# Kernel tuning notes

Hardware: AMD Instinct MI355X
Metric: run time of the kernel (lower is better)

The kernel has to match this reference:

```python
import jax, jax.numpy as jnp
import numpy as np

IN_FEATURES = 512
OUT_FEATURES = 512
GRID_SIZE = 5
SPLINE_ORDER = 3
GRID_RANGE = (-1.0, 1.0)
BATCH = 16384


def make_grid():
    h = (GRID_RANGE[1] - GRID_RANGE[0]) / GRID_SIZE
    g = jnp.arange(-SPLINE_ORDER, GRID_SIZE + SPLINE_ORDER + 1, dtype=jnp.float32) * h + GRID_RANGE[0]
    return jnp.broadcast_to(g, (IN_FEATURES, g.shape[0]))  # [in, 12]


def setup_inputs() -> dict:
    key = jax.random.key(0)
    k1, k2, k3, k4 = jax.random.split(key, 4)
    x = jax.random.normal(k1, (BATCH, IN_FEATURES), dtype=jnp.float32)
    base_weight = jax.random.normal(k2, (OUT_FEATURES, IN_FEATURES), dtype=jnp.float32) * (1.0 / np.sqrt(IN_FEATURES))
    spline_weight = jax.random.normal(k3, (OUT_FEATURES, IN_FEATURES, GRID_SIZE + SPLINE_ORDER), dtype=jnp.float32) * 0.02
    spline_scaler = jax.random.normal(k4, (OUT_FEATURES, IN_FEATURES), dtype=jnp.float32) * (1.0 / np.sqrt(IN_FEATURES))
    grid = make_grid()
    return {"x": x, "base_weight": base_weight, "spline_weight": spline_weight,
            "spline_scaler": spline_scaler, "grid": grid}


def b_splines(x, grid):
    # x: [B, in], grid: [in, G+2k+1] -> bases: [B, in, G+k]
    xe = x[:, :, None]
    bases = ((xe >= grid[:, :-1]) & (xe < grid[:, 1:])).astype(x.dtype)
    for k in range(1, SPLINE_ORDER + 1):
        left = (xe - grid[:, :-(k + 1)]) / (grid[:, k:-1] - grid[:, :-(k + 1)])
        right = (grid[:, k + 1:] - xe) / (grid[:, k + 1:] - grid[:, 1:-k])
        bases = left * bases[:, :, :-1] + right * bases[:, :, 1:]
    return bases


def reference(x, base_weight, spline_weight, spline_scaler, grid):
    B = x.shape[0]
    base_out = jax.nn.silu(x) @ base_weight.T  # [B, out]
    bases = b_splines(x, grid)  # [B, in, G+k]
    scaled_w = spline_weight * spline_scaler[:, :, None]  # [out, in, G+k]
    spline_out = bases.reshape(B, -1) @ scaled_w.reshape(OUT_FEATURES, -1).T  # [B, out]
    return base_out + spline_out
```

## Files before the change

### kernel.cpp

```cpp
#include <hip/hip_runtime.h>

typedef unsigned short u16;
typedef unsigned int u32;
typedef unsigned long long u64;
typedef __attribute__((ext_vector_type(4))) float f32x4;
typedef __attribute__((ext_vector_type(8))) float f32x8;
typedef __attribute__((ext_vector_type(8))) u16 u16x8;
typedef __attribute__((ext_vector_type(8))) __bf16 bf16x8;

#define IN_F 512
#define OUT_F 512
#define BM 64
#define NKT 72
#define NSIL 8

__device__ __forceinline__ u16 f2bf(float f) {
  u32 u = __float_as_uint(f);
  return (u16)((u + 0x7FFFu + ((u >> 16) & 1u)) >> 16);
}
__device__ __forceinline__ float siluf(float v) { return v / (1.0f + __expf(-v)); }

__device__ __forceinline__ void spline8(float xv, u64& lo, u64& hi) {
  float u = fmaf(xv, 2.5f, 5.5f);
  float cf = floorf(u);
  float f = u - cf;
  int c = (int)cf;
  bool valid = (u >= 0.0f) && (u < 11.0f);
  c = c < 0 ? 0 : (c > 10 ? 10 : c);
  float f2 = f * f, f3 = f2 * f;
  float v1 = 1.0f - f;
  float w0 = v1 * v1 * v1 * (1.0f / 6.0f);
  float w1 = 0.5f * f3 - f2 + (2.0f / 3.0f);
  float w2 = -0.5f * f3 + 0.5f * f2 + 0.5f * f + (1.0f / 6.0f);
  float w3 = f3 * (1.0f / 6.0f);
  u64 W = (u64)f2bf(w0) | ((u64)f2bf(w1) << 16) | ((u64)f2bf(w2) << 32) |
          ((u64)f2bf(w3) << 48);
  if (!valid) W = 0;
  const int s = c * 16 - 48;
  if (s < 0)       { lo = W >> (-s); hi = 0; }
  else if (s == 0) { lo = W;         hi = 0; }
  else if (s < 64) { lo = W << s;    hi = W >> (64 - s); }
  else             { lo = 0;         hi = W << (s - 64); }
}

__global__ __launch_bounds__(256) void kan_prep(const float* __restrict__ bw,
                                                const float* __restrict__ sw,
                                                const float* __restrict__ ss,
                                                u16* __restrict__ Wf) {
  const int t = blockIdx.x * 256 + threadIdx.x;
  const int o = t & 511, i = t >> 9;
  const float s = ss[(size_t)o * 512 + i];
  const float* sp = sw + ((size_t)o * 512 + i) * 8;
  f32x4 s0 = *(const f32x4*)sp;
  f32x4 s1 = *(const f32x4*)(sp + 4);
  u16x8 p;
#pragma unroll
  for (int e = 0; e < 4; ++e) {
    p[e] = f2bf(s0[e] * s);
    p[4 + e] = f2bf(s1[e] * s);
  }
  const int g = 64 + i;
  *(u16x8*)&Wf[((size_t)(g >> 2) * 32 + (o >> 4)) * 512 + (g & 3) * 128 + (o & 15) * 8] = p;
  if (i < 64) {
    const float* bp = bw + (size_t)o * 512 + i * 8;
    f32x4 b0 = *(const f32x4*)bp;
    f32x4 b1 = *(const f32x4*)(bp + 4);
    u16x8 q;
#pragma unroll
    for (int e = 0; e < 4; ++e) {
      q[e] = f2bf(b0[e]);
      q[4 + e] = f2bf(b1[e]);
    }
    *(u16x8*)&Wf[((size_t)(i >> 2) * 32 + (o >> 4)) * 512 + (i & 3) * 128 + (o & 15) * 8] = q;
  }
}

__global__ __launch_bounds__(256, 2) void kan_gemm(const float* __restrict__ x,
                                                   const u16* __restrict__ Wf,
                                                   float* __restrict__ out) {
  __shared__ u16 As[2][8 * 64 * 8];
  const int tid = threadIdx.x;
  const int b = blockIdx.x;
  const int nh = (b >> 2) & 1;
  const int n0 = nh * 256;
  const int m0 = ((b & 3) | ((b >> 3) << 2)) * BM;

  const int lane = tid & 63;
  const int wv = tid >> 6;
  const int lr = lane & 15;
  const int lk = lane >> 4;

  const u16* bbase = Wf + (size_t)(nh * 16 + wv * 4) * 512 + lane * 8;

  const int oct = tid & 7;
  const int rr = tid >> 3;
  const float* xr0 = x + (size_t)(m0 + rr) * IN_F;
  const float* xr1 = xr0 + (size_t)32 * IN_F;
  const int w0off = rr * 64 + (oct ^ (rr & 7)) * 8;
  const int w1off = w0off + 32 * 64;

  const int ro0 = lr * 64 + ((lk) ^ (lr & 7)) * 8;
  const int ro1 = lr * 64 + ((4 + lk) ^ (lr & 7)) * 8;

  f32x4 acc[4][4];
  const f32x4 zero = {0.0f, 0.0f, 0.0f, 0.0f};
#pragma unroll
  for (int m = 0; m < 4; ++m)
#pragma unroll
    for (int n = 0; n < 4; ++n) acc[m][n] = zero;

  bf16x8 brA[8], brB[8];
  float xvA0, xvA1, xvB0, xvB1;
  f32x8 xsA0, xsA1, xsB0, xsB1;

#define LOADB(REG, KT)                                                         \
  {                                                                            \
    const u16* p_ = bbase + (size_t)(KT) * 32768;                              \
    _Pragma("unroll") for (int s_ = 0; s_ < 2; ++s_)                           \
      _Pragma("unroll") for (int n_ = 0; n_ < 4; ++n_)                         \
        REG[s_ * 4 + n_] = *(const bf16x8*)(p_ + (s_ * 32 + n_) * 512);        \
  }

#define APRE(XV0, XV1, XS0, XS1, KT)                                           \
  if ((KT) < NSIL) {                                                           \
    XS0 = *(const f32x8*)(xr0 + (KT) * 64 + oct * 8);                          \
    XS1 = *(const f32x8*)(xr1 + (KT) * 64 + oct * 8);                          \
  } else {                                                                     \
    XV0 = xr0[(KT) * 8 - 64 + oct];                                            \
    XV1 = xr1[(KT) * 8 - 64 + oct];                                            \
  }

#define AWRITE(BUF, KT, XV0, XV1, XS0, XS1)                                    \
  if ((KT) < NSIL) {                                                           \
    u16x8 p0_, p1_;                                                            \
    _Pragma("unroll") for (int e_ = 0; e_ < 8; ++e_) {                         \
      p0_[e_] = f2bf(siluf(XS0[e_]));                                          \
      p1_[e_] = f2bf(siluf(XS1[e_]));                                          \
    }                                                                          \
    *(u16x8*)&As[BUF][w0off] = p0_;                                            \
    *(u16x8*)&As[BUF][w1off] = p1_;                                            \
  } else {                                                                     \
    u64 lo_, hi_;                                                              \
    union { struct { u64 a, b; } q; u16x8 v; } uu_;                            \
    spline8(XV0, lo_, hi_);                                                    \
    uu_.q.a = lo_; uu_.q.b = hi_;                                              \
    *(u16x8*)&As[BUF][w0off] = uu_.v;                                          \
    spline8(XV1, lo_, hi_);                                                    \
    uu_.q.a = lo_; uu_.q.b = hi_;                                              \
    *(u16x8*)&As[BUF][w1off] = uu_.v;                                          \
  }

#define READAF(AF, BUF, RO)                                                    \
  _Pragma("unroll") for (int m_ = 0; m_ < 4; ++m_)                             \
    AF[m_] = *(const bf16x8*)&As[BUF][(RO) + m_ * 1024];

#define MFMAS(AF, BREG, SB)                                                    \
  __builtin_amdgcn_s_setprio(1);                                               \
  _Pragma("unroll") for (int m_ = 0; m_ < 4; ++m_)                             \
    _Pragma("unroll") for (int n_ = 0; n_ < 4; ++n_)                           \
      acc[m_][n_] = __builtin_amdgcn_mfma_f32_16x16x32_bf16(                   \
          AF[m_], BREG[(SB) + n_], acc[m_][n_], 0, 0, 0);                      \
  __builtin_amdgcn_s_setprio(0);

  APRE(xvA0, xvA1, xsA0, xsA1, 0);
  LOADB(brA, 0);
  AWRITE(0, 0, xvA0, xvA1, xsA0, xsA1);
  APRE(xvA0, xvA1, xsA0, xsA1, 1);
  __syncthreads();

  for (int kt = 0; kt < NKT; kt += 2) {
    {
      bf16x8 af0[4], af1[4];
      LOADB(brB, kt + 1);
      READAF(af0, 0, ro0);
      AWRITE(1, kt + 1, xvA0, xvA1, xsA0, xsA1);
      if (kt + 2 < NKT) { APRE(xvB0, xvB1, xsB0, xsB1, kt + 2); }
      MFMAS(af0, brA, 0);
      READAF(af1, 0, ro1);
      MFMAS(af1, brA, 4);
    }
    __syncthreads();
    {
      bf16x8 af0[4], af1[4];
      if (kt + 2 < NKT) { LOADB(brA, kt + 2); }
      READAF(af0, 1, ro0);
      if (kt + 2 < NKT) { AWRITE(0, kt + 2, xvB0, xvB1, xsB0, xsB1); }
      if (kt + 3 < NKT) { APRE(xvA0, xvA1, xsA0, xsA1, kt + 3); }
      MFMAS(af0, brB, 0);
      READAF(af1, 1, ro1);
      MFMAS(af1, brB, 4);
    }
    __syncthreads();
  }

#pragma unroll
  for (int m = 0; m < 4; ++m)
#pragma unroll
    for (int n = 0; n < 4; ++n)
#pragma unroll
      for (int j = 0; j < 4; ++j)
        out[(size_t)(m0 + m * 16 + lk * 4 + j) * OUT_F + n0 + wv * 64 + n * 16 + lr] =
            acc[m][n][j];

#undef LOADB
#undef APRE
#undef AWRITE
#undef READAF
#undef MFMAS
}

extern "C" void kernel_launch(void* const* d_in, const int* in_sizes, int n_in,
                              void* d_out, int out_size, void* d_ws, size_t ws_size,
                              hipStream_t stream) {
  const float* x  = (const float*)d_in[0];
  const float* bw = (const float*)d_in[1];
  const float* sw = (const float*)d_in[2];
  const float* ss = (const float*)d_in[3];
  u16* Wf = (u16*)d_ws;

  kan_prep<<<dim3(OUT_F * IN_F / 256), 256, 0, stream>>>(bw, sw, ss, Wf);
  kan_gemm<<<dim3(512), 256, 0, stream>>>(x, Wf, (float*)d_out);
}
```

Measured before the change: 188.0 us.

## Run spline part of KAN GEMM in FP8 with scaled weights, SiLU part in BF16

```diff
diff --git a/kernel.cpp b/kernel.cpp
--- a/kernel.cpp
+++ b/kernel.cpp
@@ -1,18 +1,23 @@
 #include <hip/hip_runtime.h>
 
+typedef unsigned char u8;
 typedef unsigned short u16;
 typedef unsigned int u32;
 typedef unsigned long long u64;
 typedef __attribute__((ext_vector_type(4))) float f32x4;
 typedef __attribute__((ext_vector_type(8))) float f32x8;
+typedef __attribute__((ext_vector_type(4))) u16 u16x4;
 typedef __attribute__((ext_vector_type(8))) u16 u16x8;
+typedef __attribute__((ext_vector_type(2))) u64 u64x2;
 typedef __attribute__((ext_vector_type(8))) __bf16 bf16x8;
 
 #define IN_F 512
 #define OUT_F 512
 #define BM 64
-#define NKT 72
+#define NSPL 64
 #define NSIL 8
+#define WSCALE 64.0f
+#define WDESCALE 0.015625f
 
 __device__ __forceinline__ u16 f2bf(float f) {
   u32 u = __float_as_uint(f);
@@ -20,65 +25,98 @@
 }
 __device__ __forceinline__ float siluf(float v) { return v / (1.0f + __expf(-v)); }
 
-__device__ __forceinline__ void spline8(float xv, u64& lo, u64& hi) {
+__device__ __forceinline__ u32 cvtpk_fp8(float a, float b) {
+  u32 d;
+  asm("v_cvt_pk_fp8_f32 %0, %1, %2" : "=v"(d) : "v"(a), "v"(b));
+  return d & 0xFFFFu;
+}
+
+__device__ __forceinline__ u64 spl8f8(float xv) {
   float u = fmaf(xv, 2.5f, 5.5f);
   float cf = floorf(u);
   float f = u - cf;
   int c = (int)cf;
   bool valid = (u >= 0.0f) && (u < 11.0f);
   c = c < 0 ? 0 : (c > 10 ? 10 : c);
-  float f2 = f * f, f3 = f2 * f;
-  float v1 = 1.0f - f;
+  float f2 = f * f, f3 = f2 * f, v1 = 1.0f - f;
   float w0 = v1 * v1 * v1 * (1.0f / 6.0f);
   float w1 = 0.5f * f3 - f2 + (2.0f / 3.0f);
   float w2 = -0.5f * f3 + 0.5f * f2 + 0.5f * f + (1.0f / 6.0f);
   float w3 = f3 * (1.0f / 6.0f);
-  u64 W = (u64)f2bf(w0) | ((u64)f2bf(w1) << 16) | ((u64)f2bf(w2) << 32) |
-          ((u64)f2bf(w3) << 48);
-  if (!valid) W = 0;
-  const int s = c * 16 - 48;
-  if (s < 0)       { lo = W >> (-s); hi = 0; }
-  else if (s == 0) { lo = W;         hi = 0; }
-  else if (s < 64) { lo = W << s;    hi = W >> (64 - s); }
-  else             { lo = 0;         hi = W << (s - 64); }
+  u32 lo = cvtpk_fp8(w0, w1), hi = cvtpk_fp8(w2, w3);
+  u64 W = ((u64)(lo | (hi << 16))) << 24;
+  int sh = (6 - c) * 8;
+  u64 r = (sh >= 0) ? (W >> sh) : (W << (-sh));
+  return valid ? r : 0ull;
 }
 
 __global__ __launch_bounds__(256) void kan_prep(const float* __restrict__ bw,
                                                 const float* __restrict__ sw,
                                                 const float* __restrict__ ss,
-                                                u16* __restrict__ Wf) {
-  const int t = blockIdx.x * 256 + threadIdx.x;
-  const int o = t & 511, i = t >> 9;
-  const float s = ss[(size_t)o * 512 + i];
-  const float* sp = sw + ((size_t)o * 512 + i) * 8;
-  f32x4 s0 = *(const f32x4*)sp;
-  f32x4 s1 = *(const f32x4*)(sp + 4);
-  u16x8 p;
-#pragma unroll
-  for (int e = 0; e < 4; ++e) {
-    p[e] = f2bf(s0[e] * s);
-    p[4 + e] = f2bf(s1[e] * s);
-  }
-  const int g = 64 + i;
-  *(u16x8*)&Wf[((size_t)(g >> 2) * 32 + (o >> 4)) * 512 + (g & 3) * 128 + (o & 15) * 8] = p;
-  if (i < 64) {
-    const float* bp = bw + (size_t)o * 512 + i * 8;
-    f32x4 b0 = *(const f32x4*)bp;
-    f32x4 b1 = *(const f32x4*)(bp + 4);
-    u16x8 q;
-#pragma unroll
-    for (int e = 0; e < 4; ++e) {
-      q[e] = f2bf(b0[e]);
-      q[4 + e] = f2bf(b1[e]);
-    }
-    *(u16x8*)&Wf[((size_t)(i >> 2) * 32 + (o >> 4)) * 512 + (i & 3) * 128 + (o & 15) * 8] = q;
+                                                u8* __restrict__ Wf8,
+                                                u16* __restrict__ Wf16) {
+  __shared__ u8 PL[17152];
+  const int tid = threadIdx.x;
+  const int b = blockIdx.x;
+  if (b < 128) {
+    const int og = b & 31, ib = b >> 5;
+    const int o_loc = tid >> 4, seg = tid & 15;
+    const int orow = og * 16 + o_loc;
+    const float* swp = sw + ((size_t)orow * 512 + ib * 128) * 8 + seg * 64;
+    const float* ssp = ss + (size_t)orow * 512 + ib * 128;
+    u8* L8 = PL;
+#pragma unroll
+    for (int q = 0; q < 16; ++q) {
+      f32x4 v = *(const f32x4*)(swp + q * 4);
+      const int el = seg * 64 + q * 4;
+      float sv = ssp[el >> 3] * WSCALE;
+      u32 lo = cvtpk_fp8(v[0] * sv, v[1] * sv);
+      u32 hi = cvtpk_fp8(v[2] * sv, v[3] * sv);
+      *(u32*)&L8[o_loc * 1048 + el] = lo | (hi << 16);
+    }
+    __syncthreads();
+    const int s16 = tid & 31;
+    const int o15a = (s16 * 2) & 15, lkv = (s16 * 2) >> 4;
+#pragma unroll
+    for (int cp = 0; cp < 4; ++cp) {
+      const int stq_loc = cp * 8 + (tid >> 5);
+      const int i_loc = stq_loc * 4 + lkv;
+      u64 d0 = *(const u64*)&L8[o15a * 1048 + i_loc * 8];
+      u64 d1 = *(const u64*)&L8[(o15a + 1) * 1048 + i_loc * 8];
+      u64x2 dd = {d0, d1};
+      *(u64x2*)&Wf8[(size_t)((ib * 32 + stq_loc) * 32 + og) * 512 + s16 * 16] = dd;
+    }
+  } else {
+    const int og = b - 128;
+    u16* L16 = (u16*)PL;
+#pragma unroll
+    for (int p = 0; p < 8; ++p) {
+      const int flat = tid * 4 + p * 1024;
+      const int o_loc = flat >> 9, k = flat & 511;
+      f32x4 v = *(const f32x4*)(bw + (size_t)(og * 16 + o_loc) * 512 + k);
+      u16x4 h;
+#pragma unroll
+      for (int e = 0; e < 4; ++e) h[e] = f2bf(v[e]);
+      *(u16x4*)&L16[o_loc * 536 + k] = h;
+    }
+    __syncthreads();
+    const int s = tid & 63;
+    const int o15 = s & 15, g3 = s >> 4;
+#pragma unroll
+    for (int cp = 0; cp < 4; ++cp) {
+      const int gq = cp * 4 + (tid >> 6);
+      u16x8 d = *(const u16x8*)&L16[o15 * 536 + (gq * 4 + g3) * 8];
+      *(u16x8*)&Wf16[(size_t)(gq * 32 + og) * 512 + s * 8] = d;
+    }
   }
 }
 
 __global__ __launch_bounds__(256, 2) void kan_gemm(const float* __restrict__ x,
-                                                   const u16* __restrict__ Wf,
+                                                   const u8* __restrict__ Wf8,
+                                                   const u16* __restrict__ Wf16,
                                                    float* __restrict__ out) {
-  __shared__ u16 As[2][8 * 64 * 8];
+  __shared__ u16 As16[2][4096];
+  __shared__ u8 As8[2][4096];
   const int tid = threadIdx.x;
   const int b = blockIdx.x;
   const int nh = (b >> 2) & 1;
@@ -90,16 +128,14 @@
   const int lr = lane & 15;
   const int lk = lane >> 4;
 
-  const u16* bbase = Wf + (size_t)(nh * 16 + wv * 4) * 512 + lane * 8;
-
-  const int oct = tid & 7;
-  const int rr = tid >> 3;
+  const u8* b8base = Wf8 + (size_t)(nh * 16 + wv * 4) * 512 + lane * 8;
+  const u16* b16base = Wf16 + (size_t)(nh * 16 + wv * 4) * 512 + lane * 8;
+
+  const int oct = tid & 7, rr = tid >> 3;
   const float* xr0 = x + (size_t)(m0 + rr) * IN_F;
   const float* xr1 = xr0 + (size_t)32 * IN_F;
-  const int w0off = rr * 64 + (oct ^ (rr & 7)) * 8;
-  const int w1off = w0off + 32 * 64;
-
-  const int ro0 = lr * 64 + ((lk) ^ (lr & 7)) * 8;
+  const int woff = rr * 64 + (oct ^ (rr & 7)) * 8;
+  const int ro0 = lr * 64 + (lk ^ (lr & 7)) * 8;
   const int ro1 = lr * 64 + ((4 + lk) ^ (lr & 7)) * 8;
 
   f32x4 acc[4][4];
@@ -109,52 +145,79 @@
 #pragma unroll
     for (int n = 0; n < 4; ++n) acc[m][n] = zero;
 
-  bf16x8 brA[8], brB[8];
-  float xvA0, xvA1, xvB0, xvB1;
+  u64 b8A[8], b8B[8];
+  bf16x8 brA16[8], brB16[8];
+  float xpA0, xpA1, xpB0, xpB1;
   f32x8 xsA0, xsA1, xsB0, xsB1;
 
-#define LOADB(REG, KT)                                                         \
-  {                                                                            \
-    const u16* p_ = bbase + (size_t)(KT) * 32768;                              \
+#define BAR()                                              \
+  {                                                        \
+    asm volatile("s_waitcnt lgkmcnt(0)" ::: "memory");     \
+    __builtin_amdgcn_s_barrier();                          \
+  }
+
+#define LOADB8(REG, ST)                                                        \
+  {                                                                            \
+    const u8* p_ = b8base + (size_t)(ST)*32768;                                \
     _Pragma("unroll") for (int s_ = 0; s_ < 2; ++s_)                           \
       _Pragma("unroll") for (int n_ = 0; n_ < 4; ++n_)                         \
-        REG[s_ * 4 + n_] = *(const bf16x8*)(p_ + (s_ * 32 + n_) * 512);        \
-  }
-
-#define APRE(XV0, XV1, XS0, XS1, KT)                                           \
-  if ((KT) < NSIL) {                                                           \
-    XS0 = *(const f32x8*)(xr0 + (KT) * 64 + oct * 8);                          \
-    XS1 = *(const f32x8*)(xr1 + (KT) * 64 + oct * 8);                          \
-  } else {                                                                     \
-    XV0 = xr0[(KT) * 8 - 64 + oct];                                            \
-    XV1 = xr1[(KT) * 8 - 64 + oct];                                            \
-  }
-
-#define AWRITE(BUF, KT, XV0, XV1, XS0, XS1)                                    \
-  if ((KT) < NSIL) {                                                           \
+        REG[s_ * 4 + n_] = *(const u64*)(p_ + s_ * 16384 + n_ * 512);          \
+  }
+
+#define LOADB16(REG, KT)                                                       \
+  {                                                                            \
+    const u16* p_ = b16base + (size_t)(KT)*32768;                              \
+    _Pragma("unroll") for (int s_ = 0; s_ < 2; ++s_)                           \
+      _Pragma("unroll") for (int n_ = 0; n_ < 4; ++n_)                         \
+        REG[s_ * 4 + n_] = *(const bf16x8*)(p_ + s_ * 16384 + n_ * 512);       \
+  }
+
+#define APRE_SPL(X0, X1, ST)                                                   \
+  {                                                                            \
+    X0 = xr0[(ST)*8 + oct];                                                    \
+    X1 = xr1[(ST)*8 + oct];                                                    \
+  }
+
+#define AWRITE_SPL(BUF, X0, X1)                                                \
+  {                                                                            \
+    *(u64*)&As8[BUF][woff] = spl8f8(X0);                                       \
+    *(u64*)&As8[BUF][woff + 2048] = spl8f8(X1);                                \
+  }
+
+#define APRE_SIL(XS0, XS1, KT)                                                 \
+  {                                                                            \
+    XS0 = *(const f32x8*)(xr0 + (KT)*64 + oct * 8);                            \
+    XS1 = *(const f32x8*)(xr1 + (KT)*64 + oct * 8);                            \
+  }
+
+#define AWRITE_SIL(BUF, XS0, XS1)                                              \
+  {                                                                            \
     u16x8 p0_, p1_;                                                            \
     _Pragma("unroll") for (int e_ = 0; e_ < 8; ++e_) {                         \
       p0_[e_] = f2bf(siluf(XS0[e_]));                                          \
       p1_[e_] = f2bf(siluf(XS1[e_]));                                          \
     }                                                                          \
-    *(u16x8*)&As[BUF][w0off] = p0_;                                            \
-    *(u16x8*)&As[BUF][w1off] = p1_;                                            \
-  } else {                                                                     \
-    u64 lo_, hi_;                                                              \
-    union { struct { u64 a, b; } q; u16x8 v; } uu_;                            \
-    spline8(XV0, lo_, hi_);                                                    \
-    uu_.q.a = lo_; uu_.q.b = hi_;                                              \
-    *(u16x8*)&As[BUF][w0off] = uu_.v;                                          \
-    spline8(XV1, lo_, hi_);                                                    \
-    uu_.q.a = lo_; uu_.q.b = hi_;                                              \
-    *(u16x8*)&As[BUF][w1off] = uu_.v;                                          \
-  }
-
-#define READAF(AF, BUF, RO)                                                    \
+    *(u16x8*)&As16[BUF][woff] = p0_;                                           \
+    *(u16x8*)&As16[BUF][woff + 2048] = p1_;                                    \
+  }
+
+#define READ8(AF, BUF, RO)                                                     \
   _Pragma("unroll") for (int m_ = 0; m_ < 4; ++m_)                             \
-    AF[m_] = *(const bf16x8*)&As[BUF][(RO) + m_ * 1024];
-
-#define MFMAS(AF, BREG, SB)                                                    \
+      AF[m_] = *(const u64*)&As8[BUF][(RO) + m_ * 1024];
+
+#define READ16(AF, BUF, RO)                                                    \
+  _Pragma("unroll") for (int m_ = 0; m_ < 4; ++m_)                             \
+      AF[m_] = *(const bf16x8*)&As16[BUF][(RO) + m_ * 1024];
+
+#define MFMA8(AF, BREG, SB)                                                    \
+  __builtin_amdgcn_s_setprio(1);                                               \
+  _Pragma("unroll") for (int m_ = 0; m_ < 4; ++m_)                             \
+    _Pragma("unroll") for (int n_ = 0; n_ < 4; ++n_)                           \
+      acc[m_][n_] = __builtin_amdgcn_mfma_f32_16x16x32_fp8_fp8(                \
+          (long)AF[m_], (long)BREG[(SB) + n_], acc[m_][n_], 0, 0, 0);          \
+  __builtin_amdgcn_s_setprio(0);
+
+#define MFMA16(AF, BREG, SB)                                                   \
   __builtin_amdgcn_s_setprio(1);                                               \
   _Pragma("unroll") for (int m_ = 0; m_ < 4; ++m_)                             \
     _Pragma("unroll") for (int n_ = 0; n_ < 4; ++n_)                           \
@@ -162,36 +225,68 @@
           AF[m_], BREG[(SB) + n_], acc[m_][n_], 0, 0, 0);                      \
   __builtin_amdgcn_s_setprio(0);
 
-  APRE(xvA0, xvA1, xsA0, xsA1, 0);
-  LOADB(brA, 0);
-  AWRITE(0, 0, xvA0, xvA1, xsA0, xsA1);
-  APRE(xvA0, xvA1, xsA0, xsA1, 1);
-  __syncthreads();
-
-  for (int kt = 0; kt < NKT; kt += 2) {
+  APRE_SPL(xpA0, xpA1, 0);
+  LOADB8(b8A, 0);
+  AWRITE_SPL(0, xpA0, xpA1);
+  APRE_SPL(xpB0, xpB1, 1);
+  BAR();
+
+  for (int st = 0; st < NSPL; st += 2) {
     {
-      bf16x8 af0[4], af1[4];
-      LOADB(brB, kt + 1);
-      READAF(af0, 0, ro0);
-      AWRITE(1, kt + 1, xvA0, xvA1, xsA0, xsA1);
-      if (kt + 2 < NKT) { APRE(xvB0, xvB1, xsB0, xsB1, kt + 2); }
-      MFMAS(af0, brA, 0);
-      READAF(af1, 0, ro1);
-      MFMAS(af1, brA, 4);
-    }
-    __syncthreads();
+      u64 af0[4], af1[4];
+      LOADB8(b8B, st + 1);
+      READ8(af0, 0, ro0);
+      AWRITE_SPL(1, xpB0, xpB1);
+      if (st + 2 < NSPL) { APRE_SPL(xpA0, xpA1, st + 2); }
+      MFMA8(af0, b8A, 0);
+      READ8(af1, 0, ro1);
+      MFMA8(af1, b8A, 4);
+    }
+    BAR();
     {
-      bf16x8 af0[4], af1[4];
-      if (kt + 2 < NKT) { LOADB(brA, kt + 2); }
-      READAF(af0, 1, ro0);
-      if (kt + 2 < NKT) { AWRITE(0, kt + 2, xvB0, xvB1, xsB0, xsB1); }
-      if (kt + 3 < NKT) { APRE(xvA0, xvA1, xsA0, xsA1, kt + 3); }
-      MFMAS(af0, brB, 0);
-      READAF(af1, 1, ro1);
-      MFMAS(af1, brB, 4);
-    }
-    __syncthreads();
-  }
+      u64 af0[4], af1[4];
+      if (st + 2 < NSPL) { LOADB8(b8A, st + 2); }
+      else { LOADB16(brA16, 0); }
+      READ8(af0, 1, ro0);
+      if (st + 2 < NSPL) { AWRITE_SPL(0, xpA0, xpA1); }
+      if (st + 3 < NSPL) { APRE_SPL(xpB0, xpB1, st + 3); }
+      else if (st + 2 >= NSPL) { APRE_SIL(xsA0, xsA1, 0); }
+      MFMA8(af0, b8B, 0);
+      READ8(af1, 1, ro1);
+      MFMA8(af1, b8B, 4);
+    }
+    BAR();
+  }
+
+  AWRITE_SIL(0, xsA0, xsA1);
+  APRE_SIL(xsB0, xsB1, 1);
+#pragma unroll
+  for (int m = 0; m < 4; ++m)
+#pragma unroll
+    for (int n = 0; n < 4; ++n) acc[m][n] *= WDESCALE;
+  BAR();
+
+#define SIL_PHASE(KT, CB, CBREG, NBREG, SRC0, SRC1, TGT0, TGT1)                \
+  {                                                                            \
+    bf16x8 af0[4], af1[4];                                                     \
+    if ((KT) < 7) { LOADB16(NBREG, (KT) + 1); }                                \
+    READ16(af0, CB, ro0);                                                      \
+    if ((KT) < 7) { AWRITE_SIL(((KT) + 1) & 1, SRC0, SRC1); }                  \
+    if ((KT) < 6) { APRE_SIL(TGT0, TGT1, (KT) + 2); }                          \
+    MFMA16(af0, CBREG, 0);                                                     \
+    READ16(af1, CB, ro1);                                                      \
+    MFMA16(af1, CBREG, 4);                                                     \
+    if ((KT) < 7) BAR();                                                       \
+  }
+
+  SIL_PHASE(0, 0, brA16, brB16, xsB0, xsB1, xsA0, xsA1);
+  SIL_PHASE(1, 1, brB16, brA16, xsA0, xsA1, xsB0, xsB1);
+  SIL_PHASE(2, 0, brA16, brB16, xsB0, xsB1, xsA0, xsA1);
+  SIL_PHASE(3, 1, brB16, brA16, xsA0, xsA1, xsB0, xsB1);
+  SIL_PHASE(4, 0, brA16, brB16, xsB0, xsB1, xsA0, xsA1);
+  SIL_PHASE(5, 1, brB16, brA16, xsA0, xsA1, xsB0, xsB1);
+  SIL_PHASE(6, 0, brA16, brB16, xsB0, xsB1, xsA0, xsA1);
+  SIL_PHASE(7, 1, brB16, brA16, xsA0, xsA1, xsB0, xsB1);
 
 #pragma unroll
   for (int m = 0; m < 4; ++m)
@@ -202,11 +297,18 @@
         out[(size_t)(m0 + m * 16 + lk * 4 + j) * OUT_F + n0 + wv * 64 + n * 16 + lr] =
             acc[m][n][j];
 
-#undef LOADB
-#undef APRE
-#undef AWRITE
-#undef READAF
-#undef MFMAS
+#undef BAR
+#undef LOADB8
+#undef LOADB16
+#undef APRE_SPL
+#undef AWRITE_SPL
+#undef APRE_SIL
+#undef AWRITE_SIL
+#undef READ8
+#undef READ16
+#undef MFMA8
+#undef MFMA16
+#undef SIL_PHASE
 }
 
 extern "C" void kernel_launch(void* const* d_in, const int* in_sizes, int n_in,
@@ -216,8 +318,9 @@
   const float* bw = (const float*)d_in[1];
   const float* sw = (const float*)d_in[2];
   const float* ss = (const float*)d_in[3];
-  u16* Wf = (u16*)d_ws;
-
-  kan_prep<<<dim3(OUT_F * IN_F / 256), 256, 0, stream>>>(bw, sw, ss, Wf);
-  kan_gemm<<<dim3(512), 256, 0, stream>>>(x, Wf, (float*)d_out);
-}
+  u8* Wf8 = (u8*)d_ws;
+  u16* Wf16 = (u16*)((u8*)d_ws + (2u << 20));
+
+  kan_prep<<<dim3(160), 256, 0, stream>>>(bw, sw, ss, Wf8, Wf16);
+  kan_gemm<<<dim3(512), 256, 0, stream>>>(x, Wf8, Wf16, (float*)d_out);
+}
```

Result: faster. 168.1 us (-10.6%).
